# Optimization experiments

Hardware: AMD Instinct MI355X
Metric: run time of the kernel (lower is better)

Reference implementation:

```python
import jax, jax.numpy as jnp
import numpy as np

B, C, H, W = 2, 192, 256, 256
HEADS = 6


def _conv1x1(x, w, b):
    # x: [b,ci,h,w], w: [co,ci,1,1], b: [co]
    return jnp.einsum('oi,bihw->bohw', w[:, :, 0, 0], x) + b[None, :, None, None]


def _dwconv3x3(x, w, b):
    # depthwise 3x3, padding=1; x: [b,c,h,w], w: [c,1,3,3], b: [c]
    y = jax.lax.conv_general_dilated(
        x, w, window_strides=(1, 1), padding='SAME',
        feature_group_count=x.shape[1],
        dimension_numbers=('NCHW', 'OIHW', 'NCHW'))
    return y + b[None, :, None, None]


def _l2norm(t, eps=1e-12):
    # F.normalize(dim=-1): x / max(||x||_2, eps)
    n = jnp.sqrt(jnp.sum(t * t, axis=-1, keepdims=True))
    return t / jnp.maximum(n, eps)


def setup_inputs() -> dict:
    key = jax.random.key(0)
    ks = jax.random.split(key, 12)
    s = 0.02
    return {
        'feat_guide': jax.random.normal(ks[0], (B, C, H, W), jnp.float32),
        'feat_op': jax.random.normal(ks[1], (B, C, H, W), jnp.float32),
        'q_w': jax.random.normal(ks[2], (C, C, 1, 1), jnp.float32) * s,
        'q_b': jax.random.normal(ks[3], (C,), jnp.float32) * s,
        'kv_w': jax.random.normal(ks[4], (2 * C, C, 1, 1), jnp.float32) * s,
        'kv_b': jax.random.normal(ks[5], (2 * C,), jnp.float32) * s,
        'q_dw_w': jax.random.normal(ks[6], (C, 1, 3, 3), jnp.float32) * s,
        'q_dw_b': jax.random.normal(ks[7], (C,), jnp.float32) * s,
        'kv_dw_w': jax.random.normal(ks[8], (2 * C, 1, 3, 3), jnp.float32) * s,
        'kv_dw_b': jax.random.normal(ks[9], (2 * C,), jnp.float32) * s,
        'proj_w': jax.random.normal(ks[10], (C, C, 1, 1), jnp.float32) * s,
        'proj_b': jax.random.normal(ks[11], (C,), jnp.float32) * s,
        'temperature': jnp.ones((HEADS, 1, 1), jnp.float32),
    }


def reference(feat_guide, feat_op, q_w, q_b, kv_w, kv_b, q_dw_w, q_dw_b,
              kv_dw_w, kv_dw_b, proj_w, proj_b, temperature):
    b, c, h, w = feat_guide.shape
    q = _dwconv3x3(_conv1x1(feat_guide, q_w, q_b), q_dw_w, q_dw_b)
    kv = _dwconv3x3(_conv1x1(feat_op, kv_w, kv_b), kv_dw_w, kv_dw_b)
    k, v = jnp.split(kv, 2, axis=1)

    def heads(t):  # [b,c,h,w] -> [b,heads,c/heads,hw]
        return t.reshape(b, HEADS, c // HEADS, h * w)

    q = _l2norm(heads(q))
    k = _l2norm(heads(k))
    v = heads(v)
    # channel-wise attention: [b,heads,c',c'] scores over hw
    attn = jnp.einsum('bhcn,bhdn->bhcd', q, k) * temperature[None]
    attn = jax.nn.softmax(attn, axis=-1)
    out = jnp.einsum('bhcd,bhdn->bhcn', attn, v).reshape(b, c, h, w)
    return _conv1x1(out, proj_w, proj_b)
```

## Files before the change

### kernel.cpp

```cpp
#include <hip/hip_runtime.h>

#define HW_N 65536
#define CC 192
#define NCHUNKS 128

typedef __attribute__((ext_vector_type(8))) short short8v;
typedef __attribute__((ext_vector_type(4))) float f32x4;
typedef __attribute__((ext_vector_type(4))) int int4v;

__device__ __forceinline__ float bf2f(unsigned short u) {
  union { unsigned int i; float f; } v; v.i = ((unsigned int)u) << 16; return v.f;
}
__device__ __forceinline__ unsigned short f2bf(float f) {
  union { float f; unsigned int i; } v; v.f = f;
  unsigned int r = v.i + 0x7fffu + ((v.i >> 16) & 1u);
  return (unsigned short)(r >> 16);
}

__global__ __launch_bounds__(256) void cvt_w(
    const float* __restrict__ qw, const float* __restrict__ kvw,
    unsigned short* __restrict__ Wq, unsigned short* __restrict__ Wkv) {
  const int i = (blockIdx.x * 256 + threadIdx.x) * 8;
  const float* src; unsigned short* dst; int off;
  if (i < 36864) { src = qw; dst = Wq; off = i; }
  else { src = kvw; dst = Wkv; off = i - 36864; }
  unsigned short tmp[8];
#pragma unroll
  for (int j = 0; j < 8; ++j) tmp[j] = f2bf(src[off + j]);
  *(short8v*)(dst + off) = *(short8v*)tmp;
}

template <int INF32, int OUTF32, int PERB>
__global__ __launch_bounds__(512) void conv_gemm(
    const void* __restrict__ X_, const unsigned short* __restrict__ W,
    const float* __restrict__ bias, void* __restrict__ out_,
    int Mtot, int msplit) {
  __shared__ unsigned short Bt[2][128][40];
  const int d = blockIdx.x;
  int mt, nt;
  if (msplit == 2) { mt = (d >> 3) & 1; nt = (d & 7) | ((d >> 4) << 3); }
  else { mt = 0; nt = d; }
  const int m0 = mt * 192, n0 = nt * 128;
  const int b = blockIdx.z;
  const int t = threadIdx.x;
  const int lane = t & 63, wv = t >> 6;
  const int l15 = lane & 15, lg = lane >> 4;
  const int mrow = m0 + (wv & 3) * 48;
  const int nw = (wv >> 2) * 64;
  const int n_s = lane + 64 * (wv & 1);
  const int kq = wv >> 1;
  const size_t xbase = (size_t)b * CC * (size_t)HW_N + n0 + n_s;
  const unsigned short* Wb = W + (PERB ? (size_t)b * Mtot * CC : 0);

  float stg[8];
#pragma unroll
  for (int j = 0; j < 8; ++j) {
    const size_t xi = xbase + (size_t)(kq * 8 + j) * HW_N;
    stg[j] = INF32 ? ((const float*)X_)[xi] : bf2f(((const unsigned short*)X_)[xi]);
  }
  {
    unsigned short tmp[8];
#pragma unroll
    for (int j = 0; j < 8; ++j) tmp[j] = f2bf(stg[j]);
    *(short8v*)&Bt[0][n_s][kq * 8] = *(short8v*)tmp;
  }
  __syncthreads();

  f32x4 acc[3][4] = {};
  for (int kc = 0; kc < 6; ++kc) {
    const int buf = kc & 1;
    if (kc < 5) {
#pragma unroll
      for (int j = 0; j < 8; ++j) {
        const size_t xi = xbase + (size_t)((kc + 1) * 32 + kq * 8 + j) * HW_N;
        stg[j] = INF32 ? ((const float*)X_)[xi] : bf2f(((const unsigned short*)X_)[xi]);
      }
    }
    short8v af[3], bfr[4];
    const int k0 = kc * 32 + lg * 8;
#pragma unroll
    for (int fr = 0; fr < 3; ++fr)
      af[fr] = *(const short8v*)(Wb + (size_t)(mrow + fr * 16 + l15) * CC + k0);
#pragma unroll
    for (int fc = 0; fc < 4; ++fc)
      bfr[fc] = *(const short8v*)&Bt[buf][nw + fc * 16 + l15][lg * 8];
#pragma unroll
    for (int fr = 0; fr < 3; ++fr)
#pragma unroll
      for (int fc = 0; fc < 4; ++fc)
        acc[fr][fc] = __builtin_amdgcn_mfma_f32_16x16x32_bf16(af[fr], bfr[fc], acc[fr][fc], 0, 0, 0);
    if (kc < 5) {
      unsigned short tmp[8];
#pragma unroll
      for (int j = 0; j < 8; ++j) tmp[j] = f2bf(stg[j]);
      *(short8v*)&Bt[buf ^ 1][n_s][kq * 8] = *(short8v*)tmp;
    }
    __syncthreads();
  }

  const size_t obase = (size_t)b * Mtot * (size_t)HW_N;
#pragma unroll
  for (int fr = 0; fr < 3; ++fr) {
    const int rbase = mrow + fr * 16 + lg * 4;
#pragma unroll
    for (int r = 0; r < 4; ++r) {
      const float bb = bias[rbase + r];
#pragma unroll
      for (int fc = 0; fc < 4; ++fc) {
        const size_t oi = obase + (size_t)(rbase + r) * HW_N + n0 + nw + fc * 16 + l15;
        if (OUTF32) ((float*)out_)[oi] = acc[fr][fc][r] + bb;
        else ((unsigned short*)out_)[oi] = f2bf(acc[fr][fc][r] + bb);
      }
    }
  }
}

__global__ __launch_bounds__(256) void dwconv3x3(
    const unsigned short* __restrict__ in, const float* __restrict__ w,
    const float* __restrict__ bias, unsigned short* __restrict__ out,
    int Cstride, int coff) {
  const int t = threadIdx.x;
  const int wc = (t & 31) * 8;
  const int h = blockIdx.x * 8 + (t >> 5);
  const int c = blockIdx.y, b = blockIdx.z;
  const size_t ibase = ((size_t)b * Cstride + coff + c) * (size_t)HW_N;
  const size_t obase = ((size_t)b * CC + c) * (size_t)HW_N;
  float wv9[9];
#pragma unroll
  for (int i = 0; i < 9; ++i) wv9[i] = w[(coff + c) * 9 + i];
  const float bv = bias[coff + c];
  float f[3][10];
#pragma unroll
  for (int ky = 0; ky < 3; ++ky) {
    const int hh = h + ky - 1;
    if (hh < 0 || hh > 255) {
#pragma unroll
      for (int j = 0; j < 10; ++j) f[ky][j] = 0.f;
    } else {
      const unsigned short* row = in + ibase + hh * 256;
      short8v v = *(const short8v*)(row + wc);
      f[ky][0] = (wc > 0) ? bf2f(row[wc - 1]) : 0.f;
#pragma unroll
      for (int j = 0; j < 8; ++j) f[ky][1 + j] = bf2f((unsigned short)v[j]);
      f[ky][9] = (wc < 248) ? bf2f(row[wc + 8]) : 0.f;
    }
  }
  union { short8v v; unsigned short u[8]; } o;
#pragma unroll
  for (int j = 0; j < 8; ++j) {
    float acc = bv;
#pragma unroll
    for (int ky = 0; ky < 3; ++ky)
#pragma unroll
      for (int kx = 0; kx < 3; ++kx)
        acc += wv9[ky * 3 + kx] * f[ky][j + kx];
    o.u[j] = f2bf(acc);
  }
  *(short8v*)(out + obase + h * 256 + wc) = o.v;
}

__global__ __launch_bounds__(64) void gram_kernel(
    const unsigned short* __restrict__ Q, const unsigned short* __restrict__ K,
    float* __restrict__ Gp, float* __restrict__ nqp, float* __restrict__ nkp) {
  const int lane = threadIdx.x;
  const int l15 = lane & 15, lg = lane >> 4;
  const int chunk = blockIdx.x, h = blockIdx.y, b = blockIdx.z;
  const int bh = b * 6 + h;
  const size_t base = ((size_t)b * CC + h * 32) * (size_t)HW_N;
  f32x4 acc[2][2] = {};
  float sq[2] = {0.f, 0.f}, sk[2] = {0.f, 0.f};
  const int nst = chunk * 512 + lg * 8;
  for (int ks = 0; ks < 16; ++ks) {
    const int n = nst + ks * 32;
    short8v qa[2], kb[2];
#pragma unroll
    for (int fr = 0; fr < 2; ++fr) {
      qa[fr] = *(const short8v*)(Q + base + (size_t)(fr * 16 + l15) * HW_N + n);
      kb[fr] = *(const short8v*)(K + base + (size_t)(fr * 16 + l15) * HW_N + n);
    }
#pragma unroll
    for (int fr = 0; fr < 2; ++fr)
#pragma unroll
      for (int j = 0; j < 8; ++j) {
        float a = bf2f((unsigned short)qa[fr][j]); sq[fr] += a * a;
        float c2 = bf2f((unsigned short)kb[fr][j]); sk[fr] += c2 * c2;
      }
#pragma unroll
    for (int fr = 0; fr < 2; ++fr)
#pragma unroll
      for (int fc = 0; fc < 2; ++fc)
        acc[fr][fc] = __builtin_amdgcn_mfma_f32_16x16x32_bf16(qa[fr], kb[fc], acc[fr][fc], 0, 0, 0);
  }
  float* Gb = Gp + (size_t)(chunk * 12 + bh) * 1024;
#pragma unroll
  for (int fr = 0; fr < 2; ++fr)
#pragma unroll
    for (int fc = 0; fc < 2; ++fc)
#pragma unroll
      for (int r = 0; r < 4; ++r)
        Gb[(fr * 16 + lg * 4 + r) * 32 + fc * 16 + l15] = acc[fr][fc][r];
#pragma unroll
  for (int fr = 0; fr < 2; ++fr) {
    float v = sq[fr]; v += __shfl_down(v, 32); v += __shfl_down(v, 16);
    float u = sk[fr]; u += __shfl_down(u, 32); u += __shfl_down(u, 16);
    if (lane < 16) {
      nqp[(size_t)(chunk * 12 + bh) * 32 + fr * 16 + lane] = v;
      nkp[(size_t)(chunk * 12 + bh) * 32 + fr * 16 + lane] = u;
    }
  }
}

__global__ __launch_bounds__(256) void reduce_gram(
    const float* __restrict__ Gp, const float* __restrict__ nqp, const float* __restrict__ nkp,
    float* __restrict__ G, float* __restrict__ nq, float* __restrict__ nk) {
  const int i = blockIdx.x * 256 + threadIdx.x;
  if (i < 12 * 1024) {
    float s = 0.f;
    for (int ch = 0; ch < NCHUNKS; ++ch) s += Gp[(size_t)ch * 12288 + i];
    G[i] = s;
  } else if (i < 12 * 1024 + 384) {
    const int j = i - 12 * 1024;
    float s = 0.f;
    for (int ch = 0; ch < NCHUNKS; ++ch) s += nqp[(size_t)ch * 384 + j];
    nq[j] = s;
  } else if (i < 12 * 1024 + 768) {
    const int j = i - 12 * 1024 - 384;
    float s = 0.f;
    for (int ch = 0; ch < NCHUNKS; ++ch) s += nkp[(size_t)ch * 384 + j];
    nk[j] = s;
  }
}

__global__ __launch_bounds__(256) void attn_proj(
    const float* __restrict__ G, const float* __restrict__ nq, const float* __restrict__ nk,
    const float* __restrict__ temp, const float* __restrict__ proj_w,
    unsigned short* __restrict__ Mout) {
  const int h = blockIdx.x, b = blockIdx.y;
  const int bh = b * 6 + h;
  const int t = threadIdx.x;
  __shared__ float sc[32][33];
  __shared__ float nrmq[32], nrmk[32];
  if (t < 32) nrmq[t] = fmaxf(sqrtf(nq[bh * 32 + t]), 1e-12f);
  else if (t < 64) nrmk[t - 32] = fmaxf(sqrtf(nk[bh * 32 + t - 32]), 1e-12f);
  __syncthreads();
  const float tpr = temp[h];
  for (int i = t; i < 1024; i += 256) {
    const int c = i >> 5, d = i & 31;
    sc[c][d] = G[bh * 1024 + i] * tpr / (nrmq[c] * nrmk[d]);
  }
  __syncthreads();
  if (t < 32) {
    float mx = -1e30f;
    for (int d = 0; d < 32; ++d) mx = fmaxf(mx, sc[t][d]);
    float sum = 0.f;
    for (int d = 0; d < 32; ++d) { float e = __expf(sc[t][d] - mx); sc[t][d] = e; sum += e; }
    const float inv = 1.f / sum;
    for (int d = 0; d < 32; ++d) sc[t][d] *= inv;
  }
  __syncthreads();
  for (int i = t; i < 6144; i += 256) {
    const int co = i >> 5, d = i & 31;
    float acc = 0.f;
    for (int c = 0; c < 32; ++c) acc += proj_w[co * CC + h * 32 + c] * sc[c][d];
    Mout[((size_t)b * CC + co) * CC + h * 32 + d] = f2bf(acc);
  }
}

extern "C" void kernel_launch(void* const* d_in, const int* in_sizes, int n_in,
                              void* d_out, int out_size, void* d_ws, size_t ws_size,
                              hipStream_t stream) {
  const float* fg = (const float*)d_in[0];
  const float* fo = (const float*)d_in[1];
  const float* q_w = (const float*)d_in[2];
  const float* q_b = (const float*)d_in[3];
  const float* kv_w = (const float*)d_in[4];
  const float* kv_b = (const float*)d_in[5];
  const float* q_dw_w = (const float*)d_in[6];
  const float* q_dw_b = (const float*)d_in[7];
  const float* kv_dw_w = (const float*)d_in[8];
  const float* kv_dw_b = (const float*)d_in[9];
  const float* proj_w = (const float*)d_in[10];
  const float* proj_b = (const float*)d_in[11];
  const float* temp = (const float*)d_in[12];

  char* ws = (char*)d_ws;
  unsigned short* QC  = (unsigned short*)(ws + 0);
  unsigned short* KVC = (unsigned short*)(ws + 50331648);
  unsigned short* Qb  = (unsigned short*)(ws + 150994944);
  unsigned short* Kb  = (unsigned short*)(ws + 0);
  unsigned short* Vb  = (unsigned short*)(ws + 50331648);
  float* Gp  = (float*)(ws + 201326592);
  float* nqp = (float*)(ws + 207618048);
  float* nkp = (float*)(ws + 207814656);
  float* G   = (float*)(ws + 208011264);
  float* nqv = (float*)(ws + 208060416);
  float* nkv = (float*)(ws + 208061952);
  unsigned short* Mw  = (unsigned short*)(ws + 208063488);
  unsigned short* Wq  = (unsigned short*)(ws + 208210944);
  unsigned short* Wkv = (unsigned short*)(ws + 208284672);

  cvt_w<<<dim3(54), dim3(256), 0, stream>>>(q_w, kv_w, Wq, Wkv);
  conv_gemm<1, 0, 0><<<dim3(512, 1, 2), dim3(512), 0, stream>>>(
      (const void*)fg, Wq, q_b, (void*)QC, 192, 1);
  conv_gemm<1, 0, 0><<<dim3(1024, 1, 2), dim3(512), 0, stream>>>(
      (const void*)fo, Wkv, kv_b, (void*)KVC, 384, 2);
  dwconv3x3<<<dim3(32, 192, 2), dim3(256), 0, stream>>>(QC, q_dw_w, q_dw_b, Qb, 192, 0);
  dwconv3x3<<<dim3(32, 192, 2), dim3(256), 0, stream>>>(KVC, kv_dw_w, kv_dw_b, Kb, 384, 0);
  dwconv3x3<<<dim3(32, 192, 2), dim3(256), 0, stream>>>(KVC, kv_dw_w, kv_dw_b, Vb, 384, 192);
  gram_kernel<<<dim3(NCHUNKS, 6, 2), dim3(64), 0, stream>>>(Qb, Kb, Gp, nqp, nkp);
  reduce_gram<<<dim3(51), dim3(256), 0, stream>>>(Gp, nqp, nkp, G, nqv, nkv);
  attn_proj<<<dim3(6, 2), dim3(256), 0, stream>>>(G, nqv, nkv, temp, proj_w, Mw);
  conv_gemm<0, 1, 1><<<dim3(512, 1, 2), dim3(512), 0, stream>>>(
      (const void*)Vb, Mw, proj_b, d_out, 192, 1);
}
```

Measured before the change: 311.3 us.

## Vectorize conv GEMM loads, stage epilogue through LDS, merge dwconv launches

The 1x1-conv GEMM now loads input with 4-wide vector loads packed as bf16 pairs, and writes results through an LDS staging tile so each thread issues wide contiguous global stores. The three depthwise-conv launches are merged into one kernel indexed over 576 channel slots. This targets poor store coalescing and launch overhead. The fp32 output path is now rounded through bf16 before storing, and the extra shared memory may lower occupancy.

```diff
diff --git a/kernel.cpp b/kernel.cpp
--- a/kernel.cpp
+++ b/kernel.cpp
@@ -5,8 +5,8 @@
 #define NCHUNKS 128
 
 typedef __attribute__((ext_vector_type(8))) short short8v;
+typedef __attribute__((ext_vector_type(4))) short short4v;
 typedef __attribute__((ext_vector_type(4))) float f32x4;
-typedef __attribute__((ext_vector_type(4))) int int4v;
 
 __device__ __forceinline__ float bf2f(unsigned short u) {
   union { unsigned int i; float f; } v; v.i = ((unsigned int)u) << 16; return v.f;
@@ -36,6 +36,7 @@
     const float* __restrict__ bias, void* __restrict__ out_,
     int Mtot, int msplit) {
   __shared__ unsigned short Bt[2][128][40];
+  __shared__ unsigned short Rp[96][144];
   const int d = blockIdx.x;
   int mt, nt;
   if (msplit == 2) { mt = (d >> 3) & 1; nt = (d & 7) | ((d >> 4) << 3); }
@@ -45,37 +46,45 @@
   const int t = threadIdx.x;
   const int lane = t & 63, wv = t >> 6;
   const int l15 = lane & 15, lg = lane >> 4;
-  const int mrow = m0 + (wv & 3) * 48;
-  const int nw = (wv >> 2) * 64;
-  const int n_s = lane + 64 * (wv & 1);
-  const int kq = wv >> 1;
-  const size_t xbase = (size_t)b * CC * (size_t)HW_N + n0 + n_s;
+  const int wm = wv & 3, wn = wv >> 2;
+  const int mrow = m0 + wm * 48;
+  const int nw = wn * 64;
+  const int nq = t & 31;
+  const int kp = t >> 5;
+  const size_t xb = (size_t)b * CC * (size_t)HW_N + n0 + nq * 4;
   const unsigned short* Wb = W + (PERB ? (size_t)b * Mtot * CC : 0);
 
-  float stg[8];
-#pragma unroll
-  for (int j = 0; j < 8; ++j) {
-    const size_t xi = xbase + (size_t)(kq * 8 + j) * HW_N;
-    stg[j] = INF32 ? ((const float*)X_)[xi] : bf2f(((const unsigned short*)X_)[xi]);
-  }
-  {
-    unsigned short tmp[8];
-#pragma unroll
-    for (int j = 0; j < 8; ++j) tmp[j] = f2bf(stg[j]);
-    *(short8v*)&Bt[0][n_s][kq * 8] = *(short8v*)tmp;
-  }
+  unsigned int pk[4];
+  auto gload = [&](int kc) {
+    const size_t xo = xb + (size_t)(kc * 32 + kp * 2) * (size_t)HW_N;
+    if (INF32) {
+      f32x4 v0 = *(const f32x4*)((const float*)X_ + xo);
+      f32x4 v1 = *(const f32x4*)((const float*)X_ + xo + HW_N);
+#pragma unroll
+      for (int j = 0; j < 4; ++j)
+        pk[j] = (unsigned int)f2bf(v0[j]) | ((unsigned int)f2bf(v1[j]) << 16);
+    } else {
+      short4v a0 = *(const short4v*)((const unsigned short*)X_ + xo);
+      short4v a1 = *(const short4v*)((const unsigned short*)X_ + xo + HW_N);
+#pragma unroll
+      for (int j = 0; j < 4; ++j)
+        pk[j] = (unsigned int)(unsigned short)a0[j] | ((unsigned int)(unsigned short)a1[j] << 16);
+    }
+  };
+  auto lwrite = [&](int buf) {
+#pragma unroll
+    for (int j = 0; j < 4; ++j)
+      *(unsigned int*)&Bt[buf][nq * 4 + j][kp * 2] = pk[j];
+  };
+
+  gload(0);
+  lwrite(0);
   __syncthreads();
 
   f32x4 acc[3][4] = {};
   for (int kc = 0; kc < 6; ++kc) {
     const int buf = kc & 1;
-    if (kc < 5) {
-#pragma unroll
-      for (int j = 0; j < 8; ++j) {
-        const size_t xi = xbase + (size_t)((kc + 1) * 32 + kq * 8 + j) * HW_N;
-        stg[j] = INF32 ? ((const float*)X_)[xi] : bf2f(((const unsigned short*)X_)[xi]);
-      }
-    }
+    if (kc < 5) gload(kc + 1);
     short8v af[3], bfr[4];
     const int k0 = kc * 32 + lg * 8;
 #pragma unroll
@@ -89,46 +98,77 @@
 #pragma unroll
       for (int fc = 0; fc < 4; ++fc)
         acc[fr][fc] = __builtin_amdgcn_mfma_f32_16x16x32_bf16(af[fr], bfr[fc], acc[fr][fc], 0, 0, 0);
-    if (kc < 5) {
-      unsigned short tmp[8];
-#pragma unroll
-      for (int j = 0; j < 8; ++j) tmp[j] = f2bf(stg[j]);
-      *(short8v*)&Bt[buf ^ 1][n_s][kq * 8] = *(short8v*)tmp;
-    }
+    if (kc < 5) lwrite(buf ^ 1);
     __syncthreads();
   }
 
   const size_t obase = (size_t)b * Mtot * (size_t)HW_N;
 #pragma unroll
-  for (int fr = 0; fr < 3; ++fr) {
-    const int rbase = mrow + fr * 16 + lg * 4;
-#pragma unroll
-    for (int r = 0; r < 4; ++r) {
-      const float bb = bias[rbase + r];
-#pragma unroll
-      for (int fc = 0; fc < 4; ++fc) {
-        const size_t oi = obase + (size_t)(rbase + r) * HW_N + n0 + nw + fc * 16 + l15;
-        if (OUTF32) ((float*)out_)[oi] = acc[fr][fc][r] + bb;
-        else ((unsigned short*)out_)[oi] = f2bf(acc[fr][fc][r] + bb);
+  for (int half = 0; half < 2; ++half) {
+    if ((wm >> 1) == half) {
+      const int mbase = (wm & 1) * 48;
+#pragma unroll
+      for (int fr = 0; fr < 3; ++fr) {
+#pragma unroll
+        for (int r = 0; r < 4; ++r) {
+          const int mloc = mbase + fr * 16 + lg * 4 + r;
+          const float bb = bias[m0 + half * 96 + mloc];
+#pragma unroll
+          for (int fc = 0; fc < 4; ++fc)
+            Rp[mloc][nw + fc * 16 + l15] = f2bf(acc[fr][fc][r] + bb);
+        }
       }
     }
-  }
-}
-
-__global__ __launch_bounds__(256) void dwconv3x3(
-    const unsigned short* __restrict__ in, const float* __restrict__ w,
-    const float* __restrict__ bias, unsigned short* __restrict__ out,
-    int Cstride, int coff) {
+    __syncthreads();
+#pragma unroll
+    for (int s = 0; s < 3; ++s) {
+      const int idx = s * 512 + t;
+      const int m = idx >> 4, n8 = (idx & 15) * 8;
+      short8v v = *(short8v*)&Rp[m][n8];
+      const size_t oo = obase + (size_t)(m0 + half * 96 + m) * HW_N + n0 + n8;
+      if (OUTF32) {
+        float tmp[8];
+#pragma unroll
+        for (int j = 0; j < 8; ++j) tmp[j] = bf2f((unsigned short)v[j]);
+        *(f32x4*)((float*)out_ + oo) = *(f32x4*)&tmp[0];
+        *(f32x4*)((float*)out_ + oo + 4) = *(f32x4*)&tmp[4];
+      } else {
+        *(short8v*)((unsigned short*)out_ + oo) = v;
+      }
+    }
+    __syncthreads();
+  }
+}
+
+__global__ __launch_bounds__(256) void dwconv3x3_all(
+    const unsigned short* __restrict__ QC, const unsigned short* __restrict__ KVC,
+    const float* __restrict__ q_dw_w, const float* __restrict__ q_dw_b,
+    const float* __restrict__ kv_dw_w, const float* __restrict__ kv_dw_b,
+    unsigned short* __restrict__ Qb, unsigned short* __restrict__ Kb,
+    unsigned short* __restrict__ Vb) {
   const int t = threadIdx.x;
   const int wc = (t & 31) * 8;
   const int h = blockIdx.x * 8 + (t >> 5);
-  const int c = blockIdx.y, b = blockIdx.z;
-  const size_t ibase = ((size_t)b * Cstride + coff + c) * (size_t)HW_N;
-  const size_t obase = ((size_t)b * CC + c) * (size_t)HW_N;
+  const int y = blockIdx.y, b = blockIdx.z;
+  const unsigned short* in; const float* w; float bv; unsigned short* out;
+  if (y < 192) {
+    in = QC + ((size_t)b * 192 + y) * (size_t)HW_N;
+    w = q_dw_w + y * 9; bv = q_dw_b[y];
+    out = Qb + ((size_t)b * 192 + y) * (size_t)HW_N;
+  } else if (y < 384) {
+    const int c = y - 192;
+    in = KVC + ((size_t)b * 384 + c) * (size_t)HW_N;
+    w = kv_dw_w + c * 9; bv = kv_dw_b[c];
+    out = Kb + ((size_t)b * 192 + c) * (size_t)HW_N;
+  } else {
+    const int c = y - 384;
+    in = KVC + ((size_t)b * 384 + 192 + c) * (size_t)HW_N;
+    w = kv_dw_w + (192 + c) * 9; bv = kv_dw_b[192 + c];
+    out = Vb + ((size_t)b * 192 + c) * (size_t)HW_N;
+  }
   float wv9[9];
 #pragma unroll
-  for (int i = 0; i < 9; ++i) wv9[i] = w[(coff + c) * 9 + i];
-  const float bv = bias[coff + c];
+  for (int i = 0; i < 9; ++i) wv9[i] = w[i];
   float f[3][10];
 #pragma unroll
   for (int ky = 0; ky < 3; ++ky) {
@@ -137,7 +177,7 @@
 #pragma unroll
       for (int j = 0; j < 10; ++j) f[ky][j] = 0.f;
     } else {
-      const unsigned short* row = in + ibase + hh * 256;
+      const unsigned short* row = in + hh * 256;
       short8v v = *(const short8v*)(row + wc);
       f[ky][0] = (wc > 0) ? bf2f(row[wc - 1]) : 0.f;
 #pragma unroll
@@ -156,7 +196,7 @@
         acc += wv9[ky * 3 + kx] * f[ky][j + kx];
     o.u[j] = f2bf(acc);
   }
-  *(short8v*)(out + obase + h * 256 + wc) = o.v;
+  *(short8v*)(out + h * 256 + wc) = o.v;
 }
 
 __global__ __launch_bounds__(64) void gram_kernel(
@@ -304,9 +344,8 @@
       (const void*)fg, Wq, q_b, (void*)QC, 192, 1);
   conv_gemm<1, 0, 0><<<dim3(1024, 1, 2), dim3(512), 0, stream>>>(
       (const void*)fo, Wkv, kv_b, (void*)KVC, 384, 2);
-  dwconv3x3<<<dim3(32, 192, 2), dim3(256), 0, stream>>>(QC, q_dw_w, q_dw_b, Qb, 192, 0);
-  dwconv3x3<<<dim3(32, 192, 2), dim3(256), 0, stream>>>(KVC, kv_dw_w, kv_dw_b, Kb, 384, 0);
-  dwconv3x3<<<dim3(32, 192, 2), dim3(256), 0, stream>>>(KVC, kv_dw_w, kv_dw_b, Vb, 384, 192);
+  dwconv3x3_all<<<dim3(32, 576, 2), dim3(256), 0, stream>>>(
+      QC, KVC, q_dw_w, q_dw_b, kv_dw_w, kv_dw_b, Qb, Kb, Vb);
   gram_kernel<<<dim3(NCHUNKS, 6, 2), dim3(64), 0, stream>>>(Qb, Kb, Gp, nqp, nkp);
   reduce_gram<<<dim3(51), dim3(256), 0, stream>>>(Gp, nqp, nkp, G, nqv, nkv);
   attn_proj<<<dim3(6, 2), dim3(256), 0, stream>>>(G, nqv, nkv, temp, proj_w, Mw);
```

New measurement: 300.4 us. 1.04x faster.
